# Performance work log

Hardware: AMD Instinct MI355X
Metric: run time of the kernel (lower is better)

The kernel has to match this reference:

```python
import jax, jax.numpy as jnp
import numpy as np

N_NODES = 1_000_000
N_EDGES = 16_000_000


def setup_inputs() -> dict:
    key = jax.random.key(0)
    ks = jax.random.split(key, 12)
    feat = jax.random.normal(ks[0], (N_NODES, 1), dtype=jnp.float32)
    # symmetric GCN norm D^{-1/2}; positive values in (0, 1]
    norm = jax.random.uniform(ks[1], (N_NODES, 1), dtype=jnp.float32, minval=0.05, maxval=1.0)
    src = jax.random.randint(ks[2], (N_EDGES,), 0, N_NODES, dtype=jnp.int32)
    dst = jax.random.randint(ks[3], (N_EDGES,), 0, N_NODES, dtype=jnp.int32)
    dims = [(1, 3), (3, 3), (3, 3), (3, 3), (3, 3), (3, 1)]
    params = {}
    for i, (fi, fo) in enumerate(dims):
        w = jax.random.normal(ks[4 + i], (fi, fo), dtype=jnp.float32) * (1.0 / np.sqrt(fi))
        params[f"W{i+1}"] = w
        params[f"b{i+1}"] = jnp.zeros((fo,), dtype=jnp.float32)
    return dict(feat=feat, norm=norm, src=src, dst=dst, **params)


def _gcn_layer(h, norm, W, b, src, dst, n_nodes):
    # DGL-style GraphConv with symmetric norm:
    #   h = h * norm; agg_i = sum_{(j->i) in E} h_j; h = agg * norm; h = h @ W + b; relu
    h = h * norm                                   # [N, F]
    msgs = jnp.take(h, src, axis=0)                # [E, F] irregular gather
    agg = jax.ops.segment_sum(msgs, dst, num_segments=n_nodes)  # [N, F] scatter-add
    agg = agg * norm
    return jax.nn.relu(agg @ W + b)


def reference(feat, norm, W1, b1, W2, b2, W3, b3, W4, b4, W5, b5, W6, b6, src, dst):
    n = feat.shape[0]
    h = feat
    for W, b in ((W1, b1), (W2, b2), (W3, b3), (W4, b4), (W5, b5), (W6, b6)):
        h = _gcn_layer(h, norm, W, b, src, dst, n)
    return h  # [N, 1]
```

## Files before the change

### kernel.cpp

```cpp
#include <hip/hip_runtime.h>


#define BT 256
#define NBLK 256
#define BSHIFT 12
#define BSIZE 4096
#define LMASK 4095
#define SSH 18
#define NBINS 1024
#define M (NBLK * NBINS)
#define BTL 1024

__device__ __forceinline__ int edge_key(int s, int d) {
  return ((d >> BSHIFT) << 2) | (s >> SSH);
}

__global__ void k_init(const float* __restrict__ feat, const float* __restrict__ norm,
                       float* __restrict__ s0, int N) {
  int i = blockIdx.x * BT + threadIdx.x;
  if (i < N) s0[i] = feat[i] * norm[i];
}

__global__ void k_phist(const int* __restrict__ src, const int* __restrict__ dst,
                        int* __restrict__ histB, int E, int chunk) {
  __shared__ int h[NBINS];
  for (int i = threadIdx.x; i < NBINS; i += BT) h[i] = 0;
  __syncthreads();
  int b = blockIdx.x;
  int beg = b * chunk, end = min(beg + chunk, E);
  int i = beg + (int)threadIdx.x * 4;
  for (; i + 3 < end; i += BT * 4) {
    int4 u = *(const int4*)(src + i);
    int4 v = *(const int4*)(dst + i);
    atomicAdd(&h[edge_key(u.x, v.x)], 1);
    atomicAdd(&h[edge_key(u.y, v.y)], 1);
    atomicAdd(&h[edge_key(u.z, v.z)], 1);
    atomicAdd(&h[edge_key(u.w, v.w)], 1);
  }
  for (; i < end; ++i) atomicAdd(&h[edge_key(src[i], dst[i])], 1);
  __syncthreads();
  for (int k = threadIdx.x; k < NBINS; k += BT) histB[b * NBINS + k] = h[k];
}

__global__ void k_transp(const int* __restrict__ in, int* __restrict__ out, int R, int C) {
  __shared__ int tile[64][65];
  int c0 = blockIdx.x * 64, r0 = blockIdx.y * 64;
  int tx = threadIdx.x & 63, ty = threadIdx.x >> 6;
  for (int j = 0; j < 16; ++j) {
    int r = ty + j * 4;
    tile[r][tx] = in[(r0 + r) * C + c0 + tx];
  }
  __syncthreads();
  for (int j = 0; j < 16; ++j) {
    int r = ty + j * 4;
    out[(c0 + r) * R + r0 + tx] = tile[tx][r];
  }
}

__global__ void k_blockSum(const int* __restrict__ data, int* __restrict__ partial, int Mlen) {
  __shared__ int tmp[BT];
  int i = blockIdx.x * BT + threadIdx.x;
  tmp[threadIdx.x] = (i < Mlen) ? data[i] : 0;
  __syncthreads();
  for (int off = BT / 2; off > 0; off >>= 1) {
    if (threadIdx.x < off) tmp[threadIdx.x] += tmp[threadIdx.x + off];
    __syncthreads();
  }
  if (threadIdx.x == 0) partial[blockIdx.x] = tmp[0];
}

__global__ void k_scanPartials(int* __restrict__ partial, int nb) {
  __shared__ int tmp[BT];
  __shared__ int carry;
  int t = threadIdx.x;
  if (t == 0) carry = 0;
  __syncthreads();
  for (int base = 0; base < nb; base += BT) {
    int i = base + t;
    int v = (i < nb) ? partial[i] : 0;
    tmp[t] = v;
    __syncthreads();
    for (int off = 1; off < BT; off <<= 1) {
      int x = 0;
      if (t >= off) x = tmp[t - off];
      __syncthreads();
      tmp[t] += x;
      __syncthreads();
    }
    if (i < nb) partial[i] = tmp[t] - v + carry;
    __syncthreads();
    if (t == BT - 1) carry += tmp[BT - 1];
    __syncthreads();
  }
}

__global__ void k_scanFinal(int* __restrict__ data, const int* __restrict__ partial, int Mlen) {
  __shared__ int tmp[BT];
  int t = threadIdx.x;
  int i = blockIdx.x * BT + t;
  int v = (i < Mlen) ? data[i] : 0;
  tmp[t] = v;
  __syncthreads();
  for (int off = 1; off < BT; off <<= 1) {
    int x = 0;
    if (t >= off) x = tmp[t - off];
    __syncthreads();
    tmp[t] += x;
    __syncthreads();
  }
  if (i < Mlen) data[i] = tmp[t] - v + partial[blockIdx.x];
}

__global__ void k_pscatter(const int* __restrict__ src, const int* __restrict__ dst,
                           const int* __restrict__ scanT, unsigned int* __restrict__ packed,
                           int E, int chunk) {
  __shared__ int cur[NBINS];
  int b = blockIdx.x;
  for (int k = threadIdx.x; k < NBINS; k += BT) cur[k] = scanT[b * NBINS + k];
  __syncthreads();
  int beg = b * chunk, end = min(beg + chunk, E);
  int i = beg + (int)threadIdx.x * 4;
  for (; i + 3 < end; i += BT * 4) {
    int4 u = *(const int4*)(src + i);
    int4 v = *(const int4*)(dst + i);
    int p;
    p = atomicAdd(&cur[edge_key(u.x, v.x)], 1);
    packed[p] = ((unsigned)u.x << BSHIFT) | (unsigned)(v.x & LMASK);
    p = atomicAdd(&cur[edge_key(u.y, v.y)], 1);
    packed[p] = ((unsigned)u.y << BSHIFT) | (unsigned)(v.y & LMASK);
    p = atomicAdd(&cur[edge_key(u.z, v.z)], 1);
    packed[p] = ((unsigned)u.z << BSHIFT) | (unsigned)(v.z & LMASK);
    p = atomicAdd(&cur[edge_key(u.w, v.w)], 1);
    packed[p] = ((unsigned)u.w << BSHIFT) | (unsigned)(v.w & LMASK);
  }
  for (; i < end; ++i) {
    int p = atomicAdd(&cur[edge_key(src[i], dst[i])], 1);
    packed[p] = ((unsigned)src[i] << BSHIFT) | (unsigned)(dst[i] & LMASK);
  }
}


#define ACC3(p)                                             \
  {                                                         \
    unsigned pp = (p);                                      \
    float4 m = ((const float4*)sPrev)[pp >> BSHIFT];        \
    int loc = pp & LMASK;                                   \
    atomicAdd(&a0[loc], m.x);                               \
    atomicAdd(&a1[loc], m.y);                               \
    atomicAdd(&a2[loc], m.z);                               \
  }

#define ACC1(p)                                             \
  {                                                         \
    unsigned pp = (p);                                      \
    atomicAdd(&a[pp & LMASK], sIn[pp >> BSHIFT]);           \
  }

__global__ __launch_bounds__(BTL) void k_layer1(
    const int* __restrict__ scanT, const unsigned int* __restrict__ packed,
    const float* __restrict__ sIn, const float* __restrict__ norm,
    const float* __restrict__ W1, const float* __restrict__ b1,
    float* __restrict__ sNext, int N) {
  __shared__ float a[BSIZE];
  int k = blockIdx.x;
  for (int i = threadIdx.x; i < BSIZE; i += BTL) a[i] = 0.0f;
  int beg = scanT[k << 2], end = scanT[(k << 2) + 4];
  __syncthreads();
  int abeg = min(end, (beg + 3) & ~3);
  int t = beg + (int)threadIdx.x;
  if (t < abeg) ACC1(packed[t]);
  int i = abeg + (int)threadIdx.x * 4;
  for (; i + 3 < end; i += BTL * 4) {
    uint4 p4 = *(const uint4*)(packed + i);
    ACC1(p4.x) ACC1(p4.y) ACC1(p4.z) ACC1(p4.w)
  }
  for (; i < end; ++i) ACC1(packed[i]);
  __syncthreads();
  int node0 = k << BSHIFT;
  for (int tt = threadIdx.x; tt < BSIZE; tt += BTL) {
    int node = node0 + tt;
    if (node >= N) break;
    float n = norm[node];
    float pre = a[tt] * n;
    float h0 = fmaxf(0.0f, pre * W1[0] + b1[0]);
    float h1 = fmaxf(0.0f, pre * W1[1] + b1[1]);
    float h2 = fmaxf(0.0f, pre * W1[2] + b1[2]);
    ((float4*)sNext)[node] = make_float4(h0 * n, h1 * n, h2 * n, 0.0f);
  }
}

__global__ __launch_bounds__(BTL) void k_layer3(
    const int* __restrict__ scanT, const unsigned int* __restrict__ packed,
    const float* __restrict__ sPrev, const float* __restrict__ norm,
    const float* __restrict__ W, const float* __restrict__ bias,
    float* __restrict__ sNext, int N) {
  __shared__ float a0[BSIZE], a1[BSIZE], a2[BSIZE];
  int k = blockIdx.x;
  for (int i = threadIdx.x; i < BSIZE; i += BTL) { a0[i] = 0.0f; a1[i] = 0.0f; a2[i] = 0.0f; }
  int beg = scanT[k << 2], end = scanT[(k << 2) + 4];
  __syncthreads();
  int abeg = min(end, (beg + 3) & ~3);
  int t = beg + (int)threadIdx.x;
  if (t < abeg) ACC3(packed[t]);
  int i = abeg + (int)threadIdx.x * 4;
  for (; i + 3 < end; i += BTL * 4) {
    uint4 p4 = *(const uint4*)(packed + i);
    ACC3(p4.x) ACC3(p4.y) ACC3(p4.z) ACC3(p4.w)
  }
  for (; i < end; ++i) ACC3(packed[i]);
  __syncthreads();
  int node0 = k << BSHIFT;
  for (int tt = threadIdx.x; tt < BSIZE; tt += BTL) {
    int node = node0 + tt;
    if (node >= N) break;
    float n = norm[node];
    float x0 = a0[tt] * n, x1 = a1[tt] * n, x2 = a2[tt] * n;
    float h0 = fmaxf(0.0f, x0 * W[0] + x1 * W[3] + x2 * W[6] + bias[0]);
    float h1 = fmaxf(0.0f, x0 * W[1] + x1 * W[4] + x2 * W[7] + bias[1]);
    float h2 = fmaxf(0.0f, x0 * W[2] + x1 * W[5] + x2 * W[8] + bias[2]);
    ((float4*)sNext)[node] = make_float4(h0 * n, h1 * n, h2 * n, 0.0f);
  }
}

__global__ __launch_bounds__(BTL) void k_layer5(
    const int* __restrict__ scanT, const unsigned int* __restrict__ packed,
    const float* __restrict__ sPrev, const float* __restrict__ norm,
    const float* __restrict__ W5, const float* __restrict__ b5,
    const float* __restrict__ W6, float* __restrict__ sB, int N) {
  __shared__ float a0[BSIZE], a1[BSIZE], a2[BSIZE];
  int k = blockIdx.x;
  for (int i = threadIdx.x; i < BSIZE; i += BTL) { a0[i] = 0.0f; a1[i] = 0.0f; a2[i] = 0.0f; }
  int beg = scanT[k << 2], end = scanT[(k << 2) + 4];
  __syncthreads();
  int abeg = min(end, (beg + 3) & ~3);
  int t = beg + (int)threadIdx.x;
  if (t < abeg) ACC3(packed[t]);
  int i = abeg + (int)threadIdx.x * 4;
  for (; i + 3 < end; i += BTL * 4) {
    uint4 p4 = *(const uint4*)(packed + i);
    ACC3(p4.x) ACC3(p4.y) ACC3(p4.z) ACC3(p4.w)
  }
  for (; i < end; ++i) ACC3(packed[i]);
  __syncthreads();
  int node0 = k << BSHIFT;
  for (int tt = threadIdx.x; tt < BSIZE; tt += BTL) {
    int node = node0 + tt;
    if (node >= N) break;
    float n = norm[node];
    float x0 = a0[tt] * n, x1 = a1[tt] * n, x2 = a2[tt] * n;
    float h0 = fmaxf(0.0f, x0 * W5[0] + x1 * W5[3] + x2 * W5[6] + b5[0]);
    float h1 = fmaxf(0.0f, x0 * W5[1] + x1 * W5[4] + x2 * W5[7] + b5[1]);
    float h2 = fmaxf(0.0f, x0 * W5[2] + x1 * W5[5] + x2 * W5[8] + b5[2]);
    sB[node] = (h0 * W6[0] + h1 * W6[1] + h2 * W6[2]) * n;
  }
}

__global__ __launch_bounds__(BTL) void k_layer6(
    const int* __restrict__ scanT, const unsigned int* __restrict__ packed,
    const float* __restrict__ sIn, const float* __restrict__ norm,
    const float* __restrict__ b6, float* __restrict__ out, int N) {
  __shared__ float a[BSIZE];
  int k = blockIdx.x;
  for (int i = threadIdx.x; i < BSIZE; i += BTL) a[i] = 0.0f;
  int beg = scanT[k << 2], end = scanT[(k << 2) + 4];
  __syncthreads();
  int abeg = min(end, (beg + 3) & ~3);
  int t = beg + (int)threadIdx.x;
  if (t < abeg) ACC1(packed[t]);
  int i = abeg + (int)threadIdx.x * 4;
  for (; i + 3 < end; i += BTL * 4) {
    uint4 p4 = *(const uint4*)(packed + i);
    ACC1(p4.x) ACC1(p4.y) ACC1(p4.z) ACC1(p4.w)
  }
  for (; i < end; ++i) ACC1(packed[i]);
  __syncthreads();
  int node0 = k << BSHIFT;
  for (int tt = threadIdx.x; tt < BSIZE; tt += BTL) {
    int node = node0 + tt;
    if (node >= N) break;
    out[node] = fmaxf(0.0f, a[tt] * norm[node] + b6[0]);
  }
}

extern "C" void kernel_launch(void* const* d_in, const int* in_sizes, int n_in,
                              void* d_out, int out_size, void* d_ws, size_t ws_size,
                              hipStream_t stream) {
  const float* feat = (const float*)d_in[0];
  const float* norm = (const float*)d_in[1];
  const int* src = (const int*)d_in[2];
  const int* dst = (const int*)d_in[3];
  const float* W1 = (const float*)d_in[4];
  const float* b1 = (const float*)d_in[5];
  const float* W2 = (const float*)d_in[6];
  const float* b2 = (const float*)d_in[7];
  const float* W3 = (const float*)d_in[8];
  const float* b3 = (const float*)d_in[9];
  const float* W4 = (const float*)d_in[10];
  const float* b4 = (const float*)d_in[11];
  const float* W5 = (const float*)d_in[12];
  const float* b5 = (const float*)d_in[13];
  const float* W6 = (const float*)d_in[14];
  const float* b6 = (const float*)d_in[15];
  float* out = (float*)d_out;

  const int N = in_sizes[0];
  const int E = in_sizes[2];
  const int nbNode = (N + BT - 1) / BT;
  const int nBkt = (N + BSIZE - 1) >> BSHIFT;
  const int chunk = (((E + NBLK - 1) / NBLK) + 3) & ~3;

  unsigned int* packed = (unsigned int*)d_ws;
  int* histB = (int*)(packed + (size_t)E);
  int* histT = histB + (size_t)M;
  int* scanT = histT + (size_t)M;
  int* partial = scanT + (size_t)M;
  float* s0B = (float*)(partial + M / BT);
  float* sA = s0B + (size_t)N;
  float* sA2 = sA + (size_t)4 * N;

  k_init<<<nbNode, BT, 0, stream>>>(feat, norm, s0B, N);
  k_phist<<<NBLK, BT, 0, stream>>>(src, dst, histB, E, chunk);
  {
    dim3 g1(NBINS / 64, NBLK / 64);
    k_transp<<<g1, BT, 0, stream>>>(histB, histT, NBLK, NBINS);
  }
  k_blockSum<<<M / BT, BT, 0, stream>>>(histT, partial, M);
  k_scanPartials<<<1, BT, 0, stream>>>(partial, M / BT);
  k_scanFinal<<<M / BT, BT, 0, stream>>>(histT, partial, M);
  {
    dim3 g2(NBLK / 64, NBINS / 64);
    k_transp<<<g2, BT, 0, stream>>>(histT, scanT, NBINS, NBLK);
  }
  k_pscatter<<<NBLK, BT, 0, stream>>>(src, dst, scanT, packed, E, chunk);

  k_layer1<<<nBkt, BTL, 0, stream>>>(scanT, packed, s0B, norm, W1, b1, sA, N);
  k_layer3<<<nBkt, BTL, 0, stream>>>(scanT, packed, sA, norm, W2, b2, sA2, N);
  k_layer3<<<nBkt, BTL, 0, stream>>>(scanT, packed, sA2, norm, W3, b3, sA, N);
  k_layer3<<<nBkt, BTL, 0, stream>>>(scanT, packed, sA, norm, W4, b4, sA2, N);
  k_layer5<<<nBkt, BTL, 0, stream>>>(scanT, packed, sA2, norm, W5, b5, W6, s0B, N);
  k_layer6<<<nBkt, BTL, 0, stream>>>(scanT, packed, s0B, norm, b6, out, N);
}
```

Measured before the change: 1.547 ms.

## Split each dst bucket across two blocks with global atomic merge

```diff
diff --git a/kernel.cpp b/kernel.cpp
--- a/kernel.cpp
+++ b/kernel.cpp
@@ -1,4 +1,8 @@
 #include <hip/hip_runtime.h>
+
+#ifndef __HIP_PLATFORM_AMD__
+#define unsafeAtomicAdd atomicAdd
+#endif
 
 
 #define BT 256
@@ -19,6 +23,12 @@
                        float* __restrict__ s0, int N) {
   int i = blockIdx.x * BT + threadIdx.x;
   if (i < N) s0[i] = feat[i] * norm[i];
+}
+
+__global__ void k_zero3(float* __restrict__ a0, float* __restrict__ a1,
+                        float* __restrict__ a2, int N) {
+  int i = blockIdx.x * BT + threadIdx.x;
+  if (i < N) { a0[i] = 0.0f; a1[i] = 0.0f; a2[i] = 0.0f; }
 }
 
 __global__ void k_phist(const int* __restrict__ src, const int* __restrict__ dst,
@@ -156,130 +166,153 @@
     atomicAdd(&a[pp & LMASK], sIn[pp >> BSHIFT]);           \
   }
 
-__global__ __launch_bounds__(BTL) void k_layer1(
+__global__ __launch_bounds__(BTL) void k_edge3p(
     const int* __restrict__ scanT, const unsigned int* __restrict__ packed,
-    const float* __restrict__ sIn, const float* __restrict__ norm,
-    const float* __restrict__ W1, const float* __restrict__ b1,
-    float* __restrict__ sNext, int N) {
+    const float* __restrict__ sPrev, float* __restrict__ agg0,
+    float* __restrict__ agg1, float* __restrict__ agg2, int N) {
+  __shared__ float a0[BSIZE], a1[BSIZE], a2[BSIZE];
+  int k = blockIdx.x >> 1, h = blockIdx.x & 1;
+  for (int i = threadIdx.x; i < BSIZE; i += BTL) { a0[i] = 0.0f; a1[i] = 0.0f; a2[i] = 0.0f; }
+  int bbeg = scanT[k << 2], bend = scanT[(k << 2) + 4];
+  int mid = bbeg + ((bend - bbeg) >> 1);
+  int beg = h ? mid : bbeg;
+  int end = h ? bend : mid;
+  __syncthreads();
+  int abeg = min(end, (beg + 3) & ~3);
+  {
+    int t = beg + (int)threadIdx.x;
+    if (t < abeg) ACC3(packed[t]);
+  }
+  int i = abeg + (int)threadIdx.x * 8;
+  for (; i + 7 < end; i += BTL * 8) {
+    uint4 pa = *(const uint4*)(packed + i);
+    uint4 pb = *(const uint4*)(packed + i + 4);
+    float4 m0 = ((const float4*)sPrev)[pa.x >> BSHIFT];
+    float4 m1 = ((const float4*)sPrev)[pa.y >> BSHIFT];
+    float4 m2 = ((const float4*)sPrev)[pa.z >> BSHIFT];
+    float4 m3 = ((const float4*)sPrev)[pa.w >> BSHIFT];
+    float4 m4 = ((const float4*)sPrev)[pb.x >> BSHIFT];
+    float4 m5 = ((const float4*)sPrev)[pb.y >> BSHIFT];
+    float4 m6 = ((const float4*)sPrev)[pb.z >> BSHIFT];
+    float4 m7 = ((const float4*)sPrev)[pb.w >> BSHIFT];
+    atomicAdd(&a0[pa.x & LMASK], m0.x); atomicAdd(&a1[pa.x & LMASK], m0.y); atomicAdd(&a2[pa.x & LMASK], m0.z);
+    atomicAdd(&a0[pa.y & LMASK], m1.x); atomicAdd(&a1[pa.y & LMASK], m1.y); atomicAdd(&a2[pa.y & LMASK], m1.z);
+    atomicAdd(&a0[pa.z & LMASK], m2.x); atomicAdd(&a1[pa.z & LMASK], m2.y); atomicAdd(&a2[pa.z & LMASK], m2.z);
+    atomicAdd(&a0[pa.w & LMASK], m3.x); atomicAdd(&a1[pa.w & LMASK], m3.y); atomicAdd(&a2[pa.w & LMASK], m3.z);
+    atomicAdd(&a0[pb.x & LMASK], m4.x); atomicAdd(&a1[pb.x & LMASK], m4.y); atomicAdd(&a2[pb.x & LMASK], m4.z);
+    atomicAdd(&a0[pb.y & LMASK], m5.x); atomicAdd(&a1[pb.y & LMASK], m5.y); atomicAdd(&a2[pb.y & LMASK], m5.z);
+    atomicAdd(&a0[pb.z & LMASK], m6.x); atomicAdd(&a1[pb.z & LMASK], m6.y); atomicAdd(&a2[pb.z & LMASK], m6.z);
+    atomicAdd(&a0[pb.w & LMASK], m7.x); atomicAdd(&a1[pb.w & LMASK], m7.y); atomicAdd(&a2[pb.w & LMASK], m7.z);
+  }
+  for (; i < end; ++i) ACC3(packed[i]);
+  __syncthreads();
+  int node0 = k << BSHIFT;
+  for (int t = threadIdx.x; t < BSIZE; t += BTL) {
+    int node = node0 + t;
+    if (node < N) {
+      unsafeAtomicAdd(&agg0[node], a0[t]);
+      unsafeAtomicAdd(&agg1[node], a1[t]);
+      unsafeAtomicAdd(&agg2[node], a2[t]);
+    }
+  }
+}
+
+__global__ __launch_bounds__(BTL) void k_edge1p(
+    const int* __restrict__ scanT, const unsigned int* __restrict__ packed,
+    const float* __restrict__ sIn, float* __restrict__ agg0, int N) {
   __shared__ float a[BSIZE];
-  int k = blockIdx.x;
+  int k = blockIdx.x >> 1, h = blockIdx.x & 1;
   for (int i = threadIdx.x; i < BSIZE; i += BTL) a[i] = 0.0f;
-  int beg = scanT[k << 2], end = scanT[(k << 2) + 4];
+  int bbeg = scanT[k << 2], bend = scanT[(k << 2) + 4];
+  int mid = bbeg + ((bend - bbeg) >> 1);
+  int beg = h ? mid : bbeg;
+  int end = h ? bend : mid;
   __syncthreads();
   int abeg = min(end, (beg + 3) & ~3);
-  int t = beg + (int)threadIdx.x;
-  if (t < abeg) ACC1(packed[t]);
-  int i = abeg + (int)threadIdx.x * 4;
-  for (; i + 3 < end; i += BTL * 4) {
-    uint4 p4 = *(const uint4*)(packed + i);
-    ACC1(p4.x) ACC1(p4.y) ACC1(p4.z) ACC1(p4.w)
+  {
+    int t = beg + (int)threadIdx.x;
+    if (t < abeg) ACC1(packed[t]);
+  }
+  int i = abeg + (int)threadIdx.x * 8;
+  for (; i + 7 < end; i += BTL * 8) {
+    uint4 pa = *(const uint4*)(packed + i);
+    uint4 pb = *(const uint4*)(packed + i + 4);
+    float m0 = sIn[pa.x >> BSHIFT];
+    float m1 = sIn[pa.y >> BSHIFT];
+    float m2 = sIn[pa.z >> BSHIFT];
+    float m3 = sIn[pa.w >> BSHIFT];
+    float m4 = sIn[pb.x >> BSHIFT];
+    float m5 = sIn[pb.y >> BSHIFT];
+    float m6 = sIn[pb.z >> BSHIFT];
+    float m7 = sIn[pb.w >> BSHIFT];
+    atomicAdd(&a[pa.x & LMASK], m0);
+    atomicAdd(&a[pa.y & LMASK], m1);
+    atomicAdd(&a[pa.z & LMASK], m2);
+    atomicAdd(&a[pa.w & LMASK], m3);
+    atomicAdd(&a[pb.x & LMASK], m4);
+    atomicAdd(&a[pb.y & LMASK], m5);
+    atomicAdd(&a[pb.z & LMASK], m6);
+    atomicAdd(&a[pb.w & LMASK], m7);
   }
   for (; i < end; ++i) ACC1(packed[i]);
   __syncthreads();
   int node0 = k << BSHIFT;
-  for (int tt = threadIdx.x; tt < BSIZE; tt += BTL) {
-    int node = node0 + tt;
-    if (node >= N) break;
-    float n = norm[node];
-    float pre = a[tt] * n;
-    float h0 = fmaxf(0.0f, pre * W1[0] + b1[0]);
-    float h1 = fmaxf(0.0f, pre * W1[1] + b1[1]);
-    float h2 = fmaxf(0.0f, pre * W1[2] + b1[2]);
-    ((float4*)sNext)[node] = make_float4(h0 * n, h1 * n, h2 * n, 0.0f);
-  }
-}
-
-__global__ __launch_bounds__(BTL) void k_layer3(
-    const int* __restrict__ scanT, const unsigned int* __restrict__ packed,
-    const float* __restrict__ sPrev, const float* __restrict__ norm,
-    const float* __restrict__ W, const float* __restrict__ bias,
-    float* __restrict__ sNext, int N) {
-  __shared__ float a0[BSIZE], a1[BSIZE], a2[BSIZE];
-  int k = blockIdx.x;
-  for (int i = threadIdx.x; i < BSIZE; i += BTL) { a0[i] = 0.0f; a1[i] = 0.0f; a2[i] = 0.0f; }
-  int beg = scanT[k << 2], end = scanT[(k << 2) + 4];
-  __syncthreads();
-  int abeg = min(end, (beg + 3) & ~3);
-  int t = beg + (int)threadIdx.x;
-  if (t < abeg) ACC3(packed[t]);
-  int i = abeg + (int)threadIdx.x * 4;
-  for (; i + 3 < end; i += BTL * 4) {
-    uint4 p4 = *(const uint4*)(packed + i);
-    ACC3(p4.x) ACC3(p4.y) ACC3(p4.z) ACC3(p4.w)
-  }
-  for (; i < end; ++i) ACC3(packed[i]);
-  __syncthreads();
-  int node0 = k << BSHIFT;
-  for (int tt = threadIdx.x; tt < BSIZE; tt += BTL) {
-    int node = node0 + tt;
-    if (node >= N) break;
-    float n = norm[node];
-    float x0 = a0[tt] * n, x1 = a1[tt] * n, x2 = a2[tt] * n;
-    float h0 = fmaxf(0.0f, x0 * W[0] + x1 * W[3] + x2 * W[6] + bias[0]);
-    float h1 = fmaxf(0.0f, x0 * W[1] + x1 * W[4] + x2 * W[7] + bias[1]);
-    float h2 = fmaxf(0.0f, x0 * W[2] + x1 * W[5] + x2 * W[8] + bias[2]);
-    ((float4*)sNext)[node] = make_float4(h0 * n, h1 * n, h2 * n, 0.0f);
-  }
-}
-
-__global__ __launch_bounds__(BTL) void k_layer5(
-    const int* __restrict__ scanT, const unsigned int* __restrict__ packed,
-    const float* __restrict__ sPrev, const float* __restrict__ norm,
-    const float* __restrict__ W5, const float* __restrict__ b5,
-    const float* __restrict__ W6, float* __restrict__ sB, int N) {
-  __shared__ float a0[BSIZE], a1[BSIZE], a2[BSIZE];
-  int k = blockIdx.x;
-  for (int i = threadIdx.x; i < BSIZE; i += BTL) { a0[i] = 0.0f; a1[i] = 0.0f; a2[i] = 0.0f; }
-  int beg = scanT[k << 2], end = scanT[(k << 2) + 4];
-  __syncthreads();
-  int abeg = min(end, (beg + 3) & ~3);
-  int t = beg + (int)threadIdx.x;
-  if (t < abeg) ACC3(packed[t]);
-  int i = abeg + (int)threadIdx.x * 4;
-  for (; i + 3 < end; i += BTL * 4) {
-    uint4 p4 = *(const uint4*)(packed + i);
-    ACC3(p4.x) ACC3(p4.y) ACC3(p4.z) ACC3(p4.w)
-  }
-  for (; i < end; ++i) ACC3(packed[i]);
-  __syncthreads();
-  int node0 = k << BSHIFT;
-  for (int tt = threadIdx.x; tt < BSIZE; tt += BTL) {
-    int node = node0 + tt;
-    if (node >= N) break;
-    float n = norm[node];
-    float x0 = a0[tt] * n, x1 = a1[tt] * n, x2 = a2[tt] * n;
-    float h0 = fmaxf(0.0f, x0 * W5[0] + x1 * W5[3] + x2 * W5[6] + b5[0]);
-    float h1 = fmaxf(0.0f, x0 * W5[1] + x1 * W5[4] + x2 * W5[7] + b5[1]);
-    float h2 = fmaxf(0.0f, x0 * W5[2] + x1 * W5[5] + x2 * W5[8] + b5[2]);
-    sB[node] = (h0 * W6[0] + h1 * W6[1] + h2 * W6[2]) * n;
-  }
-}
-
-__global__ __launch_bounds__(BTL) void k_layer6(
-    const int* __restrict__ scanT, const unsigned int* __restrict__ packed,
-    const float* __restrict__ sIn, const float* __restrict__ norm,
-    const float* __restrict__ b6, float* __restrict__ out, int N) {
-  __shared__ float a[BSIZE];
-  int k = blockIdx.x;
-  for (int i = threadIdx.x; i < BSIZE; i += BTL) a[i] = 0.0f;
-  int beg = scanT[k << 2], end = scanT[(k << 2) + 4];
-  __syncthreads();
-  int abeg = min(end, (beg + 3) & ~3);
-  int t = beg + (int)threadIdx.x;
-  if (t < abeg) ACC1(packed[t]);
-  int i = abeg + (int)threadIdx.x * 4;
-  for (; i + 3 < end; i += BTL * 4) {
-    uint4 p4 = *(const uint4*)(packed + i);
-    ACC1(p4.x) ACC1(p4.y) ACC1(p4.z) ACC1(p4.w)
-  }
-  for (; i < end; ++i) ACC1(packed[i]);
-  __syncthreads();
-  int node0 = k << BSHIFT;
-  for (int tt = threadIdx.x; tt < BSIZE; tt += BTL) {
-    int node = node0 + tt;
-    if (node >= N) break;
-    out[node] = fmaxf(0.0f, a[tt] * norm[node] + b6[0]);
-  }
+  for (int t = threadIdx.x; t < BSIZE; t += BTL) {
+    int node = node0 + t;
+    if (node < N) unsafeAtomicAdd(&agg0[node], a[t]);
+  }
+}
+
+
+__global__ void k_node12(const float* __restrict__ norm, const float* __restrict__ W1,
+                         const float* __restrict__ b1, float* __restrict__ agg0,
+                         float* __restrict__ sA, int N) {
+  int i = blockIdx.x * BT + threadIdx.x;
+  if (i >= N) return;
+  float n = norm[i];
+  float pre = agg0[i] * n;
+  agg0[i] = 0.0f;
+  float h0 = fmaxf(0.0f, pre * W1[0] + b1[0]);
+  float h1 = fmaxf(0.0f, pre * W1[1] + b1[1]);
+  float h2 = fmaxf(0.0f, pre * W1[2] + b1[2]);
+  ((float4*)sA)[i] = make_float4(h0 * n, h1 * n, h2 * n, 0.0f);
+}
+
+__global__ void k_node33(const float* __restrict__ norm, const float* __restrict__ W,
+                         const float* __restrict__ bias, float* __restrict__ agg0,
+                         float* __restrict__ agg1, float* __restrict__ agg2,
+                         float* __restrict__ sNext, int N) {
+  int i = blockIdx.x * BT + threadIdx.x;
+  if (i >= N) return;
+  float n = norm[i];
+  float x0 = agg0[i] * n, x1 = agg1[i] * n, x2 = agg2[i] * n;
+  agg0[i] = 0.0f; agg1[i] = 0.0f; agg2[i] = 0.0f;
+  float h0 = fmaxf(0.0f, x0 * W[0] + x1 * W[3] + x2 * W[6] + bias[0]);
+  float h1 = fmaxf(0.0f, x0 * W[1] + x1 * W[4] + x2 * W[7] + bias[1]);
+  float h2 = fmaxf(0.0f, x0 * W[2] + x1 * W[5] + x2 * W[8] + bias[2]);
+  ((float4*)sNext)[i] = make_float4(h0 * n, h1 * n, h2 * n, 0.0f);
+}
+
+__global__ void k_node56(const float* __restrict__ norm, const float* __restrict__ W5,
+                         const float* __restrict__ b5, const float* __restrict__ W6,
+                         float* __restrict__ agg0, float* __restrict__ agg1,
+                         float* __restrict__ agg2, float* __restrict__ sB, int N) {
+  int i = blockIdx.x * BT + threadIdx.x;
+  if (i >= N) return;
+  float n = norm[i];
+  float x0 = agg0[i] * n, x1 = agg1[i] * n, x2 = agg2[i] * n;
+  agg0[i] = 0.0f; agg1[i] = 0.0f; agg2[i] = 0.0f;
+  float h0 = fmaxf(0.0f, x0 * W5[0] + x1 * W5[3] + x2 * W5[6] + b5[0]);
+  float h1 = fmaxf(0.0f, x0 * W5[1] + x1 * W5[4] + x2 * W5[7] + b5[1]);
+  float h2 = fmaxf(0.0f, x0 * W5[2] + x1 * W5[5] + x2 * W5[8] + b5[2]);
+  sB[i] = (h0 * W6[0] + h1 * W6[1] + h2 * W6[2]) * n;
+}
+
+__global__ void k_final(const float* __restrict__ norm, const float* __restrict__ b6,
+                        const float* __restrict__ agg0, float* __restrict__ out, int N) {
+  int i = blockIdx.x * BT + threadIdx.x;
+  if (i >= N) return;
+  out[i] = fmaxf(0.0f, agg0[i] * norm[i] + b6[0]);
 }
 
 extern "C" void kernel_launch(void* const* d_in, const int* in_sizes, int n_in,
@@ -317,8 +350,12 @@
   float* s0B = (float*)(partial + M / BT);
   float* sA = s0B + (size_t)N;
   float* sA2 = sA + (size_t)4 * N;
+  float* agg0 = sA2 + (size_t)4 * N;
+  float* agg1 = agg0 + (size_t)N;
+  float* agg2 = agg1 + (size_t)N;
 
   k_init<<<nbNode, BT, 0, stream>>>(feat, norm, s0B, N);
+  k_zero3<<<nbNode, BT, 0, stream>>>(agg0, agg1, agg2, N);
   k_phist<<<NBLK, BT, 0, stream>>>(src, dst, histB, E, chunk);
   {
     dim3 g1(NBINS / 64, NBLK / 64);
@@ -333,10 +370,23 @@
   }
   k_pscatter<<<NBLK, BT, 0, stream>>>(src, dst, scanT, packed, E, chunk);
 
-  k_layer1<<<nBkt, BTL, 0, stream>>>(scanT, packed, s0B, norm, W1, b1, sA, N);
-  k_layer3<<<nBkt, BTL, 0, stream>>>(scanT, packed, sA, norm, W2, b2, sA2, N);
-  k_layer3<<<nBkt, BTL, 0, stream>>>(scanT, packed, sA2, norm, W3, b3, sA, N);
-  k_layer3<<<nBkt, BTL, 0, stream>>>(scanT, packed, sA, norm, W4, b4, sA2, N);
-  k_layer5<<<nBkt, BTL, 0, stream>>>(scanT, packed, sA2, norm, W5, b5, W6, s0B, N);
-  k_layer6<<<nBkt, BTL, 0, stream>>>(scanT, packed, s0B, norm, b6, out, N);
-}
+  const int gEdge = nBkt * 2;
+
+  k_edge1p<<<gEdge, BTL, 0, stream>>>(scanT, packed, s0B, agg0, N);
+  k_node12<<<nbNode, BT, 0, stream>>>(norm, W1, b1, agg0, sA, N);
+
+  k_edge3p<<<gEdge, BTL, 0, stream>>>(scanT, packed, sA, agg0, agg1, agg2, N);
+  k_node33<<<nbNode, BT, 0, stream>>>(norm, W2, b2, agg0, agg1, agg2, sA2, N);
+
+  k_edge3p<<<gEdge, BTL, 0, stream>>>(scanT, packed, sA2, agg0, agg1, agg2, N);
+  k_node33<<<nbNode, BT, 0, stream>>>(norm, W3, b3, agg0, agg1, agg2, sA, N);
+
+  k_edge3p<<<gEdge, BTL, 0, stream>>>(scanT, packed, sA, agg0, agg1, agg2, N);
+  k_node33<<<nbNode, BT, 0, stream>>>(norm, W4, b4, agg0, agg1, agg2, sA2, N);
+
+  k_edge3p<<<gEdge, BTL, 0, stream>>>(scanT, packed, sA2, agg0, agg1, agg2, N);
+  k_node56<<<nbNode, BT, 0, stream>>>(norm, W5, b5, W6, agg0, agg1, agg2, s0B, N);
+
+  k_edge1p<<<gEdge, BTL, 0, stream>>>(scanT, packed, s0B, agg0, N);
+  k_final<<<nbNode, BT, 0, stream>>>(norm, b6, agg0, out, N);
+}
```

Measured after the change: 1.599 ms. +3.4%, slower.

## Sort edges within each dst bucket and combine runs before shared atomics

Applied to the files above, without the earlier changes.

```diff
diff --git a/kernel.cpp b/kernel.cpp
--- a/kernel.cpp
+++ b/kernel.cpp
@@ -10,9 +10,14 @@
 #define NBINS 1024
 #define M (NBLK * NBINS)
 #define BTL 1024
+#define NSB 16384
+#define CAP 64
 
 __device__ __forceinline__ int edge_key(int s, int d) {
   return ((d >> BSHIFT) << 2) | (s >> SSH);
+}
+__device__ __forceinline__ unsigned skey(unsigned p) {
+  return ((p >> 30) << 12) | (p & LMASK);
 }
 
 __global__ void k_init(const float* __restrict__ feat, const float* __restrict__ norm,
@@ -139,6 +144,67 @@
   }
 }
 
+__global__ __launch_bounds__(BTL) void k_sortB(const int* __restrict__ scanT,
+                                               unsigned int* __restrict__ packed) {
+  __shared__ int cnt[NSB / 2];
+  __shared__ int tsum[BTL];
+  int k = blockIdx.x;
+  int beg = scanT[k << 2], end = scanT[(k << 2) + 4];
+  int count = end - beg;
+  if (count > 65535) return;
+  int t = threadIdx.x;
+  for (int i = t; i < NSB / 2; i += BTL) cnt[i] = 0;
+  __syncthreads();
+  unsigned e[CAP];
+#pragma unroll
+  for (int j = 0; j < CAP; ++j) {
+    int i = beg + t + j * BTL;
+    if (i < end) {
+      unsigned p = packed[i];
+      e[j] = p;
+      unsigned kk = skey(p);
+      atomicAdd(&cnt[kk >> 1], 1 << ((kk & 1) * 16));
+    }
+  }
+  __syncthreads();
+  int base8 = t * 8;
+  int s = 0;
+#pragma unroll
+  for (int j = 0; j < 8; ++j) {
+    int pc = cnt[base8 + j];
+    s += (pc & 0xFFFF) + ((pc >> 16) & 0xFFFF);
+  }
+  tsum[t] = s;
+  __syncthreads();
+  for (int off = 1; off < BTL; off <<= 1) {
+    int x = 0;
+    if (t >= off) x = tsum[t - off];
+    __syncthreads();
+    tsum[t] += x;
+    __syncthreads();
+  }
+  int run = tsum[t] - s;
+#pragma unroll
+  for (int j = 0; j < 8; ++j) {
+    int pc = cnt[base8 + j];
+    int lo = pc & 0xFFFF, hi = (pc >> 16) & 0xFFFF;
+    cnt[base8 + j] = run | ((run + lo) << 16);
+    run += lo + hi;
+  }
+  __syncthreads();
+#pragma unroll
+  for (int j = 0; j < CAP; ++j) {
+    int i = beg + t + j * BTL;
+    if (i < end) {
+      unsigned p = e[j];
+      unsigned kk = skey(p);
+      unsigned sh = (kk & 1) * 16;
+      int old = atomicAdd(&cnt[kk >> 1], 1 << sh);
+      packed[beg + ((old >> sh) & 0xFFFF)] = p;
+    }
+  }
+}
+
 
 #define ACC3(p)                                             \
   {                                                         \
@@ -154,6 +220,25 @@
   {                                                         \
     unsigned pp = (p);                                      \
     atomicAdd(&a[pp & LMASK], sIn[pp >> BSHIFT]);           \
+  }
+
+#define STEP3(P, MM)                                        \
+  {                                                         \
+    unsigned nd = (P) & LMASK;                              \
+    if (nd == d) { r0 += MM.x; r1 += MM.y; r2 += MM.z; }    \
+    else {                                                  \
+      atomicAdd(&a0[d], r0);                                \
+      atomicAdd(&a1[d], r1);                                \
+      atomicAdd(&a2[d], r2);                                \
+      d = nd; r0 = MM.x; r1 = MM.y; r2 = MM.z;              \
+    }                                                       \
+  }
+
+#define STEP1(P, MM)                                        \
+  {                                                         \
+    unsigned nd = (P) & LMASK;                              \
+    if (nd == d) r += MM;                                   \
+    else { atomicAdd(&a[d], r); d = nd; r = MM; }           \
   }
 
 __global__ __launch_bounds__(BTL) void k_layer1(
@@ -166,13 +251,28 @@
   for (int i = threadIdx.x; i < BSIZE; i += BTL) a[i] = 0.0f;
   int beg = scanT[k << 2], end = scanT[(k << 2) + 4];
   __syncthreads();
-  int abeg = min(end, (beg + 3) & ~3);
-  int t = beg + (int)threadIdx.x;
-  if (t < abeg) ACC1(packed[t]);
-  int i = abeg + (int)threadIdx.x * 4;
-  for (; i + 3 < end; i += BTL * 4) {
-    uint4 p4 = *(const uint4*)(packed + i);
-    ACC1(p4.x) ACC1(p4.y) ACC1(p4.z) ACC1(p4.w)
+  int abeg = min(end, (beg + 7) & ~7);
+  {
+    int t = beg + (int)threadIdx.x;
+    if (t < abeg) ACC1(packed[t]);
+  }
+  int i = abeg + (int)threadIdx.x * 8;
+  for (; i + 7 < end; i += BTL * 8) {
+    uint4 pa = *(const uint4*)(packed + i);
+    uint4 pb = *(const uint4*)(packed + i + 4);
+    float m0 = sIn[pa.x >> BSHIFT];
+    float m1 = sIn[pa.y >> BSHIFT];
+    float m2 = sIn[pa.z >> BSHIFT];
+    float m3 = sIn[pa.w >> BSHIFT];
+    float m4 = sIn[pb.x >> BSHIFT];
+    float m5 = sIn[pb.y >> BSHIFT];
+    float m6 = sIn[pb.z >> BSHIFT];
+    float m7 = sIn[pb.w >> BSHIFT];
+    unsigned d = pa.x & LMASK;
+    float r = m0;
+    STEP1(pa.y, m1) STEP1(pa.z, m2) STEP1(pa.w, m3)
+    STEP1(pb.x, m4) STEP1(pb.y, m5) STEP1(pb.z, m6) STEP1(pb.w, m7)
+    atomicAdd(&a[d], r);
   }
   for (; i < end; ++i) ACC1(packed[i]);
   __syncthreads();
@@ -199,13 +299,30 @@
   for (int i = threadIdx.x; i < BSIZE; i += BTL) { a0[i] = 0.0f; a1[i] = 0.0f; a2[i] = 0.0f; }
   int beg = scanT[k << 2], end = scanT[(k << 2) + 4];
   __syncthreads();
-  int abeg = min(end, (beg + 3) & ~3);
-  int t = beg + (int)threadIdx.x;
-  if (t < abeg) ACC3(packed[t]);
-  int i = abeg + (int)threadIdx.x * 4;
-  for (; i + 3 < end; i += BTL * 4) {
-    uint4 p4 = *(const uint4*)(packed + i);
-    ACC3(p4.x) ACC3(p4.y) ACC3(p4.z) ACC3(p4.w)
+  int abeg = min(end, (beg + 7) & ~7);
+  {
+    int t = beg + (int)threadIdx.x;
+    if (t < abeg) ACC3(packed[t]);
+  }
+  int i = abeg + (int)threadIdx.x * 8;
+  for (; i + 7 < end; i += BTL * 8) {
+    uint4 pa = *(const uint4*)(packed + i);
+    uint4 pb = *(const uint4*)(packed + i + 4);
+    float4 m0 = ((const float4*)sPrev)[pa.x >> BSHIFT];
+    float4 m1 = ((const float4*)sPrev)[pa.y >> BSHIFT];
+    float4 m2 = ((const float4*)sPrev)[pa.z >> BSHIFT];
+    float4 m3 = ((const float4*)sPrev)[pa.w >> BSHIFT];
+    float4 m4 = ((const float4*)sPrev)[pb.x >> BSHIFT];
+    float4 m5 = ((const float4*)sPrev)[pb.y >> BSHIFT];
+    float4 m6 = ((const float4*)sPrev)[pb.z >> BSHIFT];
+    float4 m7 = ((const float4*)sPrev)[pb.w >> BSHIFT];
+    unsigned d = pa.x & LMASK;
+    float r0 = m0.x, r1 = m0.y, r2 = m0.z;
+    STEP3(pa.y, m1) STEP3(pa.z, m2) STEP3(pa.w, m3)
+    STEP3(pb.x, m4) STEP3(pb.y, m5) STEP3(pb.z, m6) STEP3(pb.w, m7)
+    atomicAdd(&a0[d], r0);
+    atomicAdd(&a1[d], r1);
+    atomicAdd(&a2[d], r2);
   }
   for (; i < end; ++i) ACC3(packed[i]);
   __syncthreads();
@@ -232,13 +349,30 @@
   for (int i = threadIdx.x; i < BSIZE; i += BTL) { a0[i] = 0.0f; a1[i] = 0.0f; a2[i] = 0.0f; }
   int beg = scanT[k << 2], end = scanT[(k << 2) + 4];
   __syncthreads();
-  int abeg = min(end, (beg + 3) & ~3);
-  int t = beg + (int)threadIdx.x;
-  if (t < abeg) ACC3(packed[t]);
-  int i = abeg + (int)threadIdx.x * 4;
-  for (; i + 3 < end; i += BTL * 4) {
-    uint4 p4 = *(const uint4*)(packed + i);
-    ACC3(p4.x) ACC3(p4.y) ACC3(p4.z) ACC3(p4.w)
+  int abeg = min(end, (beg + 7) & ~7);
+  {
+    int t = beg + (int)threadIdx.x;
+    if (t < abeg) ACC3(packed[t]);
+  }
+  int i = abeg + (int)threadIdx.x * 8;
+  for (; i + 7 < end; i += BTL * 8) {
+    uint4 pa = *(const uint4*)(packed + i);
+    uint4 pb = *(const uint4*)(packed + i + 4);
+    float4 m0 = ((const float4*)sPrev)[pa.x >> BSHIFT];
+    float4 m1 = ((const float4*)sPrev)[pa.y >> BSHIFT];
+    float4 m2 = ((const float4*)sPrev)[pa.z >> BSHIFT];
+    float4 m3 = ((const float4*)sPrev)[pa.w >> BSHIFT];
+    float4 m4 = ((const float4*)sPrev)[pb.x >> BSHIFT];
+    float4 m5 = ((const float4*)sPrev)[pb.y >> BSHIFT];
+    float4 m6 = ((const float4*)sPrev)[pb.z >> BSHIFT];
+    float4 m7 = ((const float4*)sPrev)[pb.w >> BSHIFT];
+    unsigned d = pa.x & LMASK;
+    float r0 = m0.x, r1 = m0.y, r2 = m0.z;
+    STEP3(pa.y, m1) STEP3(pa.z, m2) STEP3(pa.w, m3)
+    STEP3(pb.x, m4) STEP3(pb.y, m5) STEP3(pb.z, m6) STEP3(pb.w, m7)
+    atomicAdd(&a0[d], r0);
+    atomicAdd(&a1[d], r1);
+    atomicAdd(&a2[d], r2);
   }
   for (; i < end; ++i) ACC3(packed[i]);
   __syncthreads();
@@ -264,13 +398,28 @@
   for (int i = threadIdx.x; i < BSIZE; i += BTL) a[i] = 0.0f;
   int beg = scanT[k << 2], end = scanT[(k << 2) + 4];
   __syncthreads();
-  int abeg = min(end, (beg + 3) & ~3);
-  int t = beg + (int)threadIdx.x;
-  if (t < abeg) ACC1(packed[t]);
-  int i = abeg + (int)threadIdx.x * 4;
-  for (; i + 3 < end; i += BTL * 4) {
-    uint4 p4 = *(const uint4*)(packed + i);
-    ACC1(p4.x) ACC1(p4.y) ACC1(p4.z) ACC1(p4.w)
+  int abeg = min(end, (beg + 7) & ~7);
+  {
+    int t = beg + (int)threadIdx.x;
+    if (t < abeg) ACC1(packed[t]);
+  }
+  int i = abeg + (int)threadIdx.x * 8;
+  for (; i + 7 < end; i += BTL * 8) {
+    uint4 pa = *(const uint4*)(packed + i);
+    uint4 pb = *(const uint4*)(packed + i + 4);
+    float m0 = sIn[pa.x >> BSHIFT];
+    float m1 = sIn[pa.y >> BSHIFT];
+    float m2 = sIn[pa.z >> BSHIFT];
+    float m3 = sIn[pa.w >> BSHIFT];
+    float m4 = sIn[pb.x >> BSHIFT];
+    float m5 = sIn[pb.y >> BSHIFT];
+    float m6 = sIn[pb.z >> BSHIFT];
+    float m7 = sIn[pb.w >> BSHIFT];
+    unsigned d = pa.x & LMASK;
+    float r = m0;
+    STEP1(pa.y, m1) STEP1(pa.z, m2) STEP1(pa.w, m3)
+    STEP1(pb.x, m4) STEP1(pb.y, m5) STEP1(pb.z, m6) STEP1(pb.w, m7)
+    atomicAdd(&a[d], r);
   }
   for (; i < end; ++i) ACC1(packed[i]);
   __syncthreads();
@@ -332,6 +481,7 @@
     k_transp<<<g2, BT, 0, stream>>>(histT, scanT, NBINS, NBLK);
   }
   k_pscatter<<<NBLK, BT, 0, stream>>>(src, dst, scanT, packed, E, chunk);
+  k_sortB<<<nBkt, BTL, 0, stream>>>(scanT, packed);
 
   k_layer1<<<nBkt, BTL, 0, stream>>>(scanT, packed, s0B, norm, W1, b1, sA, N);
   k_layer3<<<nBkt, BTL, 0, stream>>>(scanT, packed, sA, norm, W2, b2, sA2, N);
```

Result: slower. 1.625 ms (+5.0%).
